# Performance work log

Hardware: AMD Instinct MI355X
Metric: run time of the kernel (lower is better)

The kernel has to match this reference:

```python
import jax, jax.numpy as jnp
import numpy as np

B, C, D = 4096, 128, 768
EPS = 1e-12
SEP = 4.0  # pair_dist in [0, 2], so 4.0 separates per-class key bands


def setup_inputs() -> dict:
    key = jax.random.key(0)
    k1, k2, k3, k4 = jax.random.split(key, 4)
    features = jax.random.normal(k1, (B, D), jnp.float32)
    centers = jax.random.normal(k2, (C, D), jnp.float32)
    labels = jax.random.randint(k3, (B,), 0, C, dtype=jnp.int32)
    cam_ids = jax.random.randint(k4, (B,), 0, 8, dtype=jnp.int32)
    return {"features": features, "centers": centers, "labels": labels, "cam_ids": cam_ids}


def _l2norm(x):
    return x / jnp.maximum(jnp.linalg.norm(x, axis=1, keepdims=True), EPS)


def reference(features, centers, labels, cam_ids):
    # cam_ids is unused by the original module.
    E = _l2norm(features)                         # [B, D] unit embeddings
    Cn = _l2norm(jax.lax.stop_gradient(centers))  # [C, D] unit centers (detached)

    S = E @ E.T                                   # [B, B] pairwise cosine (differentiable)
    EC = jnp.sum(E * Cn[labels], axis=1)          # [B] cosine(embedding_i, center_{label_i})

    li = labels[:, None]
    lj = labels[None, :]
    ar = jnp.arange(B)
    upper = ar[:, None] < ar[None, :]             # i < j (each unordered pair once)
    valid = (li == lj) & upper                    # within-class pairs

    # pair distances are computed under no_grad in torch -> stop_gradient
    pd = jax.lax.stop_gradient(1.0 - jnp.clip(S, -1.0, 1.0))  # [B, B]

    # per-class lower-median threshold via ONE global sort:
    # key = class_id * SEP + pair_dist groups pairs by class, sorted by dist within class
    m = jnp.zeros((C,), jnp.int32).at[labels].add(1)   # class sizes
    npairs = (m * (m - 1)) // 2                         # pairs per class
    key_mat = jnp.where(valid, li.astype(jnp.float32) * SEP + pd, jnp.inf)
    sorted_keys = jnp.sort(key_mat.ravel())             # [B*B]
    offs = jnp.cumsum(npairs) - npairs                  # start of each class segment
    med_idx = offs + jnp.maximum(npairs - 1, 0) // 2    # torch.median = lower median
    thr = sorted_keys[med_idx] - SEP * jnp.arange(C, dtype=jnp.float32)
    thr = jnp.where(npairs > 0, thr, jnp.inf)           # classes with <2 samples: no pairs

    sel = valid & (pd > thr[labels][:, None])           # strict > as in torch

    # random interpolation ratio (no_grad in torch)
    r = jax.lax.stop_gradient(jax.random.uniform(jax.random.key(1), (B, B), jnp.float32))

    # sampled = normalize(r*e_i + (1-r)*e_j); since ||e||=1:
    #   ||sampled_pre||^2 = r^2 + (1-r)^2 + 2 r (1-r) <e_i, e_j>
    #   <sampled, c> = (r <e_i,c> + (1-r) <e_j,c>) / ||sampled_pre||
    norm2 = r * r + (1.0 - r) * (1.0 - r) + 2.0 * r * (1.0 - r) * S
    norm = jnp.maximum(jnp.sqrt(jnp.maximum(norm2, 0.0)), EPS)
    dot = (r * EC[:, None] + (1.0 - r) * EC[None, :]) / norm
    dist = 1.0 - jnp.clip(dot, -1.0, 1.0)               # [B, B]

    # the torch loop iterates over every label occurrence, so a class with m_c
    # occurrences contributes its class loss (and pair count) m_c times
    w = m[labels].astype(jnp.float32)[:, None]          # weight per pair (left label's class)
    loss = jnp.sum(jnp.where(sel, w * dist, 0.0))
    nsamp = jnp.sum(jnp.where(sel, w, 0.0))
    return jnp.where(nsamp > 0, loss / nsamp, 0.0)
```

## Files before the change

### kernel.cpp

```cpp
#include <hip/hip_runtime.h>

#define B_ 4096
#define C_ 128
#define D_ 768
#define NT 1024
#define NW (NT/64)
#define M_MAX 96
#define P_MAX (M_MAX*(M_MAX-1)/2)
#define CK 128
#define NCH (D_/CK)
#define SROW 132
#define TILE_F (M_MAX*SROW)
#define LM2 2
#define RC 127
#define SPT ((M_MAX*(CK/4) + NT - 1)/NT)
#define LCAP 64

__device__ __forceinline__ float wave_red(float v){
#pragma unroll
  for (int o = 32; o > 0; o >>= 1) v += __shfl_down(v, o, 64);
  return v;
}
__device__ __forceinline__ float clamp1(float x){ return fminf(fmaxf(x, -1.f), 1.f); }
__device__ __forceinline__ unsigned rotl32(unsigned x, int r){ return (x << r) | (x >> (32 - r)); }
__device__ __forceinline__ float dot4(float4 a, float4 b){
  return fmaf(a.x, b.x, fmaf(a.y, b.y, fmaf(a.z, b.z, a.w * b.w)));
}

__device__ float rand_ij(unsigned n){
  const unsigned half = (unsigned)B_ * (unsigned)B_ / 2u;
  unsigned c0, c1; bool hi;
  if (n < half){ c0 = n; c1 = n + half; hi = false; }
  else         { c0 = n - half; c1 = n; hi = true; }
  const unsigned K0 = 0u, K1 = 1u, K2 = 0x1BD11BDBu;
  unsigned x0 = c0 + K0, x1 = c1 + K1;
#define TFR(r) { x0 += x1; x1 = rotl32(x1, (r)); x1 ^= x0; }
  TFR(13) TFR(15) TFR(26) TFR(6)  x0 += K1; x1 += K2 + 1u;
  TFR(17) TFR(29) TFR(16) TFR(24) x0 += K2; x1 += K0 + 2u;
  TFR(13) TFR(15) TFR(26) TFR(6)  x0 += K0; x1 += K1 + 3u;
  TFR(17) TFR(29) TFR(16) TFR(24) x0 += K1; x1 += K2 + 4u;
  TFR(13) TFR(15) TFR(26) TFR(6)  x0 += K2; x1 += K0 + 5u;
#undef TFR
  unsigned bits = hi ? x1 : x0;
  return __uint_as_float((bits >> 9) | 0x3F800000u) - 1.0f;
}

__device__ __forceinline__ void decode_pair(int p, int m, int* a_, int* b_){
  float fm = (float)(2*m - 1);
  int a = (int)((fm - sqrtf(fm*fm - 8.0f*(float)p)) * 0.5f);
  a = max(0, min(a, m - 2));
  while (a > 0 && (a*(2*m - 1 - a))/2 > p) --a;
  while (((a + 1)*(2*m - 2 - a))/2 <= p) ++a;
  *a_ = a;
  *b_ = a + 1 + (p - (a*(2*m - 1 - a))/2);
}

__device__ float dotg(const float* x, const float* y){
  float s = 0.f;
  for (int k = 0; k < D_; ++k) s = fmaf(x[k], y[k], s);
  return s;
}
__device__ float S_pair_g(const float* feat, int ga, int gb){
  const float* ra = feat + (size_t)ga * D_;
  const float* rb = feat + (size_t)gb * D_;
  float d = dotg(ra, rb);
  float na = 1.f / fmaxf(sqrtf(dotg(ra, ra)), 1e-12f);
  float nb = 1.f / fmaxf(sqrtf(dotg(rb, rb)), 1e-12f);
  return d * na * nb;
}

__global__ __launch_bounds__(NT) void k_all(
    const float* __restrict__ feat, const float* __restrict__ cent,
    const int* __restrict__ labels,
    float* __restrict__ lossv, float* __restrict__ wv,
    unsigned* __restrict__ flags, float* __restrict__ out)
{
  const int c = blockIdx.x;
  const int tid = threadIdx.x;
  const int wid = tid >> 6, lane = tid & 63;

  __shared__ int   gid_s[M_MAX];
  __shared__ int   mcount;
  __shared__ __align__(16) float tile[2 * TILE_F];
  __shared__ __align__(16) float cvec[2][CK];
  float*          Sl     = tile;
  unsigned short* fidx_s = (unsigned short*)(tile + P_MAX);
  __shared__ float selfs[M_MAX];
  __shared__ float ecs[M_MAX];
  __shared__ float cn_sh;
  __shared__ int   wcnt[NW * 64];
  __shared__ int   B0_sh, ex_sh, B1_sh, ex2_sh;
  __shared__ float thr_sh;
  __shared__ float lst[LCAP];
  __shared__ int   listn;
  __shared__ float redbuf[2 * NW];
  __shared__ int   last_sh;

  if (tid == 0) mcount = 0;
  __syncthreads();
  {
    const int4* lab4 = (const int4*)labels;
    for (int i = tid; i < B_ / 4; i += NT){
      int4 L = lab4[i];
      int base = i << 2;
      if (L.x == c){ int p = atomicAdd(&mcount, 1); if (p < M_MAX) gid_s[p] = base; }
      if (L.y == c){ int p = atomicAdd(&mcount, 1); if (p < M_MAX) gid_s[p] = base + 1; }
      if (L.z == c){ int p = atomicAdd(&mcount, 1); if (p < M_MAX) gid_s[p] = base + 2; }
      if (L.w == c){ int p = atomicAdd(&mcount, 1); if (p < M_MAX) gid_s[p] = base + 3; }
    }
  }
  __syncthreads();
  const int m = mcount;

  float lloss = 0.f, lw = 0.f;

  if (m >= 2 && m <= M_MAX){
    const int P = m * (m - 1) / 2;
    const int k0 = (P - 1) >> 1;
    const float wc = (float)m;
    const int nst = m * (CK / 4);

    const int h    = (m + 1) >> 1;
    const int Upair = h * (h + 1) / 2;
    const int hec  = (m + 2) >> 1;
    const int U    = Upair + hec;

    int c0[LM2], c1[LM2], c2[LM2], c3[LM2];
    int tAv[LM2], tBv[LM2];
    float acc[LM2][4];
    int nlay = 0;
#pragma unroll
    for (int t = 0; t < LM2; ++t){
      acc[t][0] = acc[t][1] = acc[t][2] = acc[t][3] = 0.f;
      c0[t] = c1[t] = c2[t] = c3[t] = 0; tAv[t] = 0; tBv[t] = -3;
      int u = tid + t * NT;
      if (u < U){
        nlay = t + 1;
        if (u < Upair){
          int ta = 0;
          while ((ta + 1) * h - ((ta + 1) * ta) / 2 <= u) ++ta;
          int tb = ta + (u - (ta * h - (ta * (ta - 1)) / 2));
          c0[t] = ta; c1[t] = ta + h; c2[t] = tb; c3[t] = tb + h;
          tAv[t] = ta; tBv[t] = tb;
        } else {
          int g = u - Upair;
          int l1 = g + hec;
          c0[t] = g;
          c1[t] = (l1 == m) ? RC : ((l1 < m) ? l1 : 0);
          c2[t] = RC; c3[t] = RC;
          tAv[t] = g; tBv[t] = -1;
        }
      }
    }

    float4 pf[SPT];
    float4 cpf;
#pragma unroll
    for (int k = 0; k < SPT; ++k){
      int e = tid + k * NT;
      if (e < nst){
        int r = e >> 5, j = e & 31;
        pf[k] = ((const float4*)(feat + (size_t)gid_s[r] * D_))[j];
      }
    }
    if (tid < CK/4) cpf = ((const float4*)(cent + (size_t)c * D_))[tid];
#pragma unroll
    for (int k = 0; k < SPT; ++k){
      int e = tid + k * NT;
      if (e < nst){
        int r = e >> 5, j = e & 31;
        ((float4*)&tile[r * SROW])[j] = pf[k];
      }
    }
    if (tid < CK/4) ((float4*)cvec[0])[tid] = cpf;
    __syncthreads();

    for (int ch = 0; ch < NCH; ++ch){
      const int cur = ch & 1;
      if (ch + 1 < NCH){
        const int d0 = (ch + 1) * CK;
#pragma unroll
        for (int k = 0; k < SPT; ++k){
          int e = tid + k * NT;
          if (e < nst){
            int r = e >> 5, j = e & 31;
            pf[k] = ((const float4*)(feat + (size_t)gid_s[r] * D_ + d0))[j];
          }
        }
        if (tid < CK/4) cpf = ((const float4*)(cent + (size_t)c * D_ + d0))[tid];
      }
      {
        const float* tl = tile + cur * TILE_F;
        const float4* cv4 = (const float4*)cvec[cur];
#pragma unroll
        for (int t = 0; t < LM2; ++t){
          if (t < nlay){
            const float4* A0 = (c0[t] == RC) ? cv4 : (const float4*)&tl[c0[t] * SROW];
            const float4* A1 = (c1[t] == RC) ? cv4 : (const float4*)&tl[c1[t] * SROW];
            const float4* Bp0 = (c2[t] == RC) ? cv4 : (const float4*)&tl[c2[t] * SROW];
            const float4* Bp1 = (c3[t] == RC) ? cv4 : (const float4*)&tl[c3[t] * SROW];
            float s00 = 0.f, s01 = 0.f, s10 = 0.f, s11 = 0.f;
#pragma unroll 8
            for (int j = 0; j < CK/4; ++j){
              float4 a0 = A0[j], a1 = A1[j], b0 = Bp0[j], b1 = Bp1[j];
              s00 += dot4(a0, b0); s01 += dot4(a0, b1);
              s10 += dot4(a1, b0); s11 += dot4(a1, b1);
            }
            acc[t][0] += s00; acc[t][1] += s01;
            acc[t][2] += s10; acc[t][3] += s11;
          }
        }
      }
      if (ch + 1 < NCH){
        float* tn = tile + (cur ^ 1) * TILE_F;
#pragma unroll
        for (int k = 0; k < SPT; ++k){
          int e = tid + k * NT;
          if (e < nst){
            int r = e >> 5, j = e & 31;
            ((float4*)&tn[r * SROW])[j] = pf[k];
          }
        }
        if (tid < CK/4) ((float4*)cvec[cur ^ 1])[tid] = cpf;
      }
      __syncthreads();
    }

#pragma unroll
    for (int t = 0; t < LM2; ++t){
      if (t < nlay){
        if (tBv[t] == -1){
          int g = tAv[t], l1 = g + hec;
          ecs[g] = acc[t][0];
          if (l1 == m) cn_sh = acc[t][2];
          else if (l1 < m) ecs[l1] = acc[t][2];
        } else if (tBv[t] >= 0){
          const int ta = tAv[t], tb = tBv[t];
          const int a1 = ta + h;
          if (ta == tb){
            if (ta < m) selfs[ta] = acc[t][0];
            if (a1 < m) selfs[a1] = acc[t][3];
          }
        }
      }
    }
    __syncthreads();
    if (tid == 0) listn = 0;
    if (tid < m){
      float rn  = 1.f / fmaxf(sqrtf(selfs[tid]), 1e-12f);
      float cno = 1.f / fmaxf(sqrtf(cn_sh), 1e-12f);
      selfs[tid] = rn;
      ecs[tid] = ecs[tid] * rn * cno;
    }
    __syncthreads();

    float pdq_[LM2][4];
    int   fq_[LM2][4];
#pragma unroll
    for (int t = 0; t < LM2; ++t){
#pragma unroll
      for (int s = 0; s < 4; ++s){ pdq_[t][s] = 0.f; fq_[t][s] = -1; }
      if (t < nlay && tBv[t] >= 0){
        const int ta = tAv[t], tb = tBv[t], a1 = ta + h, b1 = tb + h;
        const int  pa[4]  = { ta, ta, tb, a1 };
        const int  pb[4]  = { tb, b1, a1, b1 };
        const bool dif    = (ta != tb);
        const bool val[4] = { dif, b1 < m, dif && (a1 < m), dif && (a1 < m) && (b1 < m) };
#pragma unroll
        for (int s = 0; s < 4; ++s){
          if (val[s]){
            float S = acc[t][s] * selfs[pa[s]]; S *= selfs[pb[s]];
            float pd = 1.f - clamp1(S);
            int p = (pa[s] * (2*m - 1 - pa[s])) / 2 + (pb[s] - pa[s] - 1);
            Sl[p] = S;
            int f = min(4095, (int)(pd * 2048.f));
            fidx_s[p] = (unsigned short)f;
            pdq_[t][s] = pd; fq_[t][s] = f;
          }
        }
      }
    }
    __syncthreads();

    const int nch = (P + NT - 1) / NT;
    int cl = 0;
    for (int t = 0; t < nch; ++t){
      int p = tid + t * NT;
      int bkt = -1;
      if (p < P) bkt = fidx_s[p] >> 6;
#pragma unroll
      for (int k = 0; k < 64; ++k){
        unsigned long long msk = __ballot(bkt == k);
        if (lane == k) cl += __popcll(msk);
      }
    }
    wcnt[wid*64 + lane] = cl;
    __syncthreads();
    if (tid < 64){
      int tot = 0;
#pragma unroll
      for (int w = 0; w < NW; ++w) tot += wcnt[w*64 + tid];
      int inc = tot;
#pragma unroll
      for (int o = 1; o < 64; o <<= 1){
        int v = __shfl_up(inc, o, 64);
        if (tid >= o) inc += v;
      }
      int excl = inc - tot;
      if (excl <= k0 && k0 < inc){ B0_sh = tid; ex_sh = excl; }
    }
    __syncthreads();
    const int Bsel0 = B0_sh;
    const int kt = k0 - ex_sh;
    cl = 0;
    for (int t = 0; t < nch; ++t){
      int p = tid + t * NT;
      int bkt = -1;
      if (p < P){
        int f = fidx_s[p];
        if ((f >> 6) == Bsel0) bkt = f & 63;
      }
#pragma unroll
      for (int k = 0; k < 64; ++k){
        unsigned long long msk = __ballot(bkt == k);
        if (lane == k) cl += __popcll(msk);
      }
    }
    wcnt[wid*64 + lane] = cl;
    __syncthreads();
    if (tid < 64){
      int tot = 0;
#pragma unroll
      for (int w = 0; w < NW; ++w) tot += wcnt[w*64 + tid];
      int inc = tot;
#pragma unroll
      for (int o = 1; o < 64; o <<= 1){
        int v = __shfl_up(inc, o, 64);
        if (tid >= o) inc += v;
      }
      int excl = inc - tot;
      if (excl <= kt && kt < inc){ B1_sh = tid; ex2_sh = excl; }
    }
    __syncthreads();
    const int fsel = (Bsel0 << 6) | B1_sh;
    const int ktf  = kt - ex2_sh;

#pragma unroll
    for (int t = 0; t < LM2; ++t){
#pragma unroll
      for (int s = 0; s < 4; ++s){
        if (fq_[t][s] == fsel){
          int ix = atomicAdd(&listn, 1);
          if (ix < LCAP) lst[ix] = pdq_[t][s];
        }
      }
    }
    __syncthreads();
    const int ln = listn;
    if (ln <= LCAP){
      if (tid < ln){
        float pdp = lst[tid];
        int lt = 0, eq = 0;
        for (int j = 0; j < ln; ++j){
          float v = lst[j];
          lt += (v < pdp); eq += (v == pdp);
        }
        if (lt <= ktf && ktf < lt + eq) thr_sh = pdp;
      }
    } else {
      for (int p = tid; p < P; p += NT){
        if (fidx_s[p] == (unsigned short)fsel){
          float pdp = 1.f - clamp1(Sl[p]);
          int lt = 0, eq = 0;
          for (int q = 0; q < P; ++q){
            float pdq = 1.f - clamp1(Sl[q]);
            lt += (pdq < pdp); eq += (pdq == pdp);
          }
          if (lt <= k0 && k0 < lt + eq) thr_sh = pdp;
        }
      }
    }
    __syncthreads();
    const float thr = thr_sh;

    for (int p = tid; p < P; p += NT){
      float S = Sl[p];
      float pd = 1.f - clamp1(S);
      if (pd > thr){
        int a, b; decode_pair(p, m, &a, &b);
        int ga = gid_s[a], gb = gid_s[b];
        float ea = ecs[a], eb = ecs[b];
        int i, j; float eci, ecj;
        if (ga < gb){ i = ga; j = gb; eci = ea; ecj = eb; }
        else        { i = gb; j = ga; eci = eb; ecj = ea; }
        float r = rand_ij((unsigned)i * (unsigned)B_ + (unsigned)j);
        float omr = 1.f - r;
        float n2 = r * r + omr * omr + 2.f * r * omr * S;
        float nrm = fmaxf(sqrtf(fmaxf(n2, 0.f)), 1e-12f);
        float dt = clamp1((r * eci + omr * ecj) / nrm);
        lloss += wc * (1.f - dt);
        lw += wc;
      }
    }
  } else if (m > M_MAX){
    int* mem = (int*)Sl;
    if (tid == 0) B0_sh = 0;
    __syncthreads();
    for (int i = tid; i < B_; i += NT)
      if (labels[i] == c){ int p = atomicAdd(&B0_sh, 1); mem[p] = i; }
    __syncthreads();
    const int P = m * (m - 1) / 2;
    const int k0 = (P - 1) >> 1;
    const float wc = (float)m;
    const float* cc = cent + (size_t)c * D_;
    const float cno = 1.f / fmaxf(sqrtf(dotg(cc, cc)), 1e-12f);
    for (int p = tid; p < P; p += NT){
      int a, b; decode_pair(p, m, &a, &b);
      float pdp = 1.f - clamp1(S_pair_g(feat, mem[a], mem[b]));
      int lt = 0, eq = 0;
      for (int q = 0; q < P; ++q){
        int a2, b2; decode_pair(q, m, &a2, &b2);
        float pdq = 1.f - clamp1(S_pair_g(feat, mem[a2], mem[b2]));
        lt += (pdq < pdp); eq += (pdq == pdp);
      }
      if (lt <= k0 && k0 < lt + eq) thr_sh = pdp;
    }
    __syncthreads();
    const float thr = thr_sh;
    for (int p = tid; p < P; p += NT){
      int a, b; decode_pair(p, m, &a, &b);
      int ga = mem[a], gb = mem[b];
      float S = S_pair_g(feat, ga, gb);
      float pd = 1.f - clamp1(S);
      if (pd > thr){
        if (ga > gb){ int t2 = ga; ga = gb; gb = t2; }
        const float* ra = feat + (size_t)ga * D_;
        const float* rb = feat + (size_t)gb * D_;
        float eci = dotg(ra, cc) / fmaxf(sqrtf(dotg(ra, ra)), 1e-12f) * cno;
        float ecj = dotg(rb, cc) / fmaxf(sqrtf(dotg(rb, rb)), 1e-12f) * cno;
        float r = rand_ij((unsigned)ga * (unsigned)B_ + (unsigned)gb);
        float omr = 1.f - r;
        float n2 = r * r + omr * omr + 2.f * r * omr * S;
        float nrm = fmaxf(sqrtf(fmaxf(n2, 0.f)), 1e-12f);
        float dt = clamp1((r * eci + omr * ecj) / nrm);
        lloss += wc * (1.f - dt);
        lw += wc;
      }
    }
  }

  lloss = wave_red(lloss); lw = wave_red(lw);
  if (lane == 0){ redbuf[wid] = lloss; redbuf[NW + wid] = lw; }
  __syncthreads();
  if (tid == 0){
    float tl = 0.f, tw = 0.f;
#pragma unroll
    for (int i = 0; i < NW; ++i){ tl += redbuf[i]; tw += redbuf[NW + i]; }
    __hip_atomic_store(&lossv[c], tl, __ATOMIC_RELAXED, __HIP_MEMORY_SCOPE_AGENT);
    __hip_atomic_store(&wv[c],   tw, __ATOMIC_RELAXED, __HIP_MEMORY_SCOPE_AGENT);
    unsigned old = __hip_atomic_fetch_add(&flags[0], 1u, __ATOMIC_ACQ_REL,
                                          __HIP_MEMORY_SCOPE_AGENT);
    last_sh = ((old & 127u) == 127u) ? 1 : 0;
  }
  __syncthreads();
  if (last_sh){
    float lv = 0.f, wvv = 0.f;
    if (tid < C_){
      lv  = __hip_atomic_load(&lossv[tid], __ATOMIC_RELAXED, __HIP_MEMORY_SCOPE_AGENT);
      wvv = __hip_atomic_load(&wv[tid],   __ATOMIC_RELAXED, __HIP_MEMORY_SCOPE_AGENT);
    }
    lv = wave_red(lv); wvv = wave_red(wvv);
    if (lane == 0){ redbuf[wid] = lv; redbuf[NW + wid] = wvv; }
    __syncthreads();
    if (tid == 0){
      float l = redbuf[0] + redbuf[1];
      float w = redbuf[NW] + redbuf[NW + 1];
      out[0] = (w > 0.f) ? (l / w) : 0.f;
    }
  }
}

extern "C" void kernel_launch(void* const* d_in, const int* in_sizes, int n_in,
                              void* d_out, int out_size, void* d_ws, size_t ws_size,
                              hipStream_t stream)
{
  const float* feat   = (const float*)d_in[0];
  const float* cent   = (const float*)d_in[1];
  const int*   labels = (const int*)d_in[2];

  char* ws = (char*)d_ws;
  float*    lossv = (float*)(ws + 0);
  float*    wvv   = (float*)(ws + 512);
  unsigned* flags = (unsigned*)(ws + 1024);

  k_all<<<C_, NT, 0, stream>>>(feat, cent, labels, lossv, wvv, flags, (float*)d_out);
}
```

Baseline: 112.9 us.

## Load full feature rows into LDS at once for small classes

For classes with at most 48 members, the kernel now loads all 768-dim feature rows and the center into shared memory in one step. It then computes the Gram and center dot products in one pass, which removes the six-chunk double-buffered loop and its per-chunk barriers. The fine-bucket candidate list is now rebuilt by scanning the fidx_s array instead of being kept in per-thread registers, which frees registers. The larger shared buffer (about 148KB) may reduce occupancy, and the scan adds a pass over P entries.

```diff
diff --git a/kernel.cpp b/kernel.cpp
--- a/kernel.cpp
+++ b/kernel.cpp
@@ -15,6 +15,11 @@
 #define RC 127
 #define SPT ((M_MAX*(CK/4) + NT - 1)/NT)
 #define LCAP 64
+#define MCAP 48
+#define SROWF 772
+#define FLAT_F (MCAP*SROWF)
+#define SHP_F (FLAT_F + 768)
+#define SPTF 9
 
 __device__ __forceinline__ float wave_red(float v){
 #pragma unroll
@@ -81,10 +86,9 @@
 
   __shared__ int   gid_s[M_MAX];
   __shared__ int   mcount;
-  __shared__ __align__(16) float tile[2 * TILE_F];
-  __shared__ __align__(16) float cvec[2][CK];
-  float*          Sl     = tile;
-  unsigned short* fidx_s = (unsigned short*)(tile + P_MAX);
+  __shared__ __align__(16) float shp[SHP_F];
+  float*          Sl     = shp;
+  unsigned short* fidx_s = (unsigned short*)(shp + P_MAX);
   __shared__ float selfs[M_MAX];
   __shared__ float ecs[M_MAX];
   __shared__ float cn_sh;
@@ -118,169 +122,282 @@
     const int P = m * (m - 1) / 2;
     const int k0 = (P - 1) >> 1;
     const float wc = (float)m;
-    const int nst = m * (CK / 4);
-
     const int h    = (m + 1) >> 1;
-    const int Upair = h * (h + 1) / 2;
     const int hec  = (m + 2) >> 1;
-    const int U    = Upair + hec;
-
-    int c0[LM2], c1[LM2], c2[LM2], c3[LM2];
-    int tAv[LM2], tBv[LM2];
-    float acc[LM2][4];
-    int nlay = 0;
-#pragma unroll
-    for (int t = 0; t < LM2; ++t){
-      acc[t][0] = acc[t][1] = acc[t][2] = acc[t][3] = 0.f;
-      c0[t] = c1[t] = c2[t] = c3[t] = 0; tAv[t] = 0; tBv[t] = -3;
-      int u = tid + t * NT;
-      if (u < U){
-        nlay = t + 1;
-        if (u < Upair){
+
+    if (m <= MCAP){
+      const int Upair = h * (h + 1) / 2;
+      const int U = Upair + hec;
+      int uty = -1, ta_ = 0, tb_ = 0, g_ = 0;
+      int rc0 = 0, rc1 = 0, rc2 = 0, rc3 = 0;
+      if (tid < U){
+        if (tid < Upair){
           int ta = 0;
-          while ((ta + 1) * h - ((ta + 1) * ta) / 2 <= u) ++ta;
-          int tb = ta + (u - (ta * h - (ta * (ta - 1)) / 2));
-          c0[t] = ta; c1[t] = ta + h; c2[t] = tb; c3[t] = tb + h;
-          tAv[t] = ta; tBv[t] = tb;
+          while ((ta + 1) * h - ((ta + 1) * ta) / 2 <= tid) ++ta;
+          int tb = ta + (tid - (ta * h - (ta * (ta - 1)) / 2));
+          uty = 0; ta_ = ta; tb_ = tb;
+          rc0 = ta; rc1 = ta + h; rc2 = tb; rc3 = tb + h;
         } else {
-          int g = u - Upair;
-          int l1 = g + hec;
-          c0[t] = g;
-          c1[t] = (l1 == m) ? RC : ((l1 < m) ? l1 : 0);
-          c2[t] = RC; c3[t] = RC;
-          tAv[t] = g; tBv[t] = -1;
-        }
-      }
-    }
-
-    float4 pf[SPT];
-    float4 cpf;
-#pragma unroll
-    for (int k = 0; k < SPT; ++k){
-      int e = tid + k * NT;
-      if (e < nst){
-        int r = e >> 5, j = e & 31;
-        pf[k] = ((const float4*)(feat + (size_t)gid_s[r] * D_))[j];
-      }
-    }
-    if (tid < CK/4) cpf = ((const float4*)(cent + (size_t)c * D_))[tid];
-#pragma unroll
-    for (int k = 0; k < SPT; ++k){
-      int e = tid + k * NT;
-      if (e < nst){
-        int r = e >> 5, j = e & 31;
-        ((float4*)&tile[r * SROW])[j] = pf[k];
-      }
-    }
-    if (tid < CK/4) ((float4*)cvec[0])[tid] = cpf;
-    __syncthreads();
-
-    for (int ch = 0; ch < NCH; ++ch){
-      const int cur = ch & 1;
-      if (ch + 1 < NCH){
-        const int d0 = (ch + 1) * CK;
-#pragma unroll
-        for (int k = 0; k < SPT; ++k){
-          int e = tid + k * NT;
-          if (e < nst){
-            int r = e >> 5, j = e & 31;
-            pf[k] = ((const float4*)(feat + (size_t)gid_s[r] * D_ + d0))[j];
-          }
-        }
-        if (tid < CK/4) cpf = ((const float4*)(cent + (size_t)c * D_ + d0))[tid];
-      }
-      {
-        const float* tl = tile + cur * TILE_F;
-        const float4* cv4 = (const float4*)cvec[cur];
-#pragma unroll
-        for (int t = 0; t < LM2; ++t){
-          if (t < nlay){
-            const float4* A0 = (c0[t] == RC) ? cv4 : (const float4*)&tl[c0[t] * SROW];
-            const float4* A1 = (c1[t] == RC) ? cv4 : (const float4*)&tl[c1[t] * SROW];
-            const float4* Bp0 = (c2[t] == RC) ? cv4 : (const float4*)&tl[c2[t] * SROW];
-            const float4* Bp1 = (c3[t] == RC) ? cv4 : (const float4*)&tl[c3[t] * SROW];
-            float s00 = 0.f, s01 = 0.f, s10 = 0.f, s11 = 0.f;
+          int g = tid - Upair, l1 = g + hec;
+          uty = 2; g_ = g;
+          rc0 = g;
+          rc1 = (l1 == m) ? RC : ((l1 < m) ? l1 : 0);
+          rc2 = RC; rc3 = RC;
+        }
+      }
+
+      const int nstF = m * 192;
+      float4 st[SPTF];
+      float4 cvf;
+#pragma unroll
+      for (int k = 0; k < SPTF; ++k){
+        int e = tid + k * NT;
+        if (e < nstF){
+          int r = e / 192, j = e - r * 192;
+          st[k] = ((const float4*)(feat + (size_t)gid_s[r] * D_))[j];
+        }
+      }
+      if (tid < 192) cvf = ((const float4*)(cent + (size_t)c * D_))[tid];
+#pragma unroll
+      for (int k = 0; k < SPTF; ++k){
+        int e = tid + k * NT;
+        if (e < nstF){
+          int r = e / 192, j = e - r * 192;
+          ((float4*)&shp[r * SROWF])[j] = st[k];
+        }
+      }
+      if (tid < 192) ((float4*)(shp + FLAT_F))[tid] = cvf;
+      __syncthreads();
+
+      float a0s = 0.f, a1s = 0.f, a2s = 0.f, a3s = 0.f;
+      if (uty >= 0){
+        const float4* cv4 = (const float4*)(shp + FLAT_F);
+        const float4* A0 = (rc0 == RC) ? cv4 : (const float4*)&shp[rc0 * SROWF];
+        const float4* A1 = (rc1 == RC) ? cv4 : (const float4*)&shp[rc1 * SROWF];
+        const float4* Bp0 = (rc2 == RC) ? cv4 : (const float4*)&shp[rc2 * SROWF];
+        const float4* Bp1 = (rc3 == RC) ? cv4 : (const float4*)&shp[rc3 * SROWF];
+        for (int ch = 0; ch < NCH; ++ch){
+          const int q0 = ch * 32;
+          float s00 = 0.f, s01 = 0.f, s10 = 0.f, s11 = 0.f;
 #pragma unroll 8
-            for (int j = 0; j < CK/4; ++j){
-              float4 a0 = A0[j], a1 = A1[j], b0 = Bp0[j], b1 = Bp1[j];
-              s00 += dot4(a0, b0); s01 += dot4(a0, b1);
-              s10 += dot4(a1, b0); s11 += dot4(a1, b1);
+          for (int j = 0; j < 32; ++j){
+            float4 a0 = A0[q0 + j], a1 = A1[q0 + j];
+            float4 b0 = Bp0[q0 + j], b1 = Bp1[q0 + j];
+            s00 += dot4(a0, b0); s01 += dot4(a0, b1);
+            s10 += dot4(a1, b0); s11 += dot4(a1, b1);
+          }
+          a0s += s00; a1s += s01; a2s += s10; a3s += s11;
+        }
+      }
+
+      if (uty == 0){
+        if (ta_ == tb_){
+          if (ta_ < m) selfs[ta_] = a0s;
+          if (ta_ + h < m) selfs[ta_ + h] = a3s;
+        }
+      } else if (uty == 2){
+        ecs[g_] = a0s;
+        int l1 = g_ + hec;
+        if (l1 == m) cn_sh = a2s;
+        else if (l1 < m) ecs[l1] = a2s;
+      }
+      __syncthreads();
+      if (tid == 0) listn = 0;
+      if (tid < m){
+        float rn  = 1.f / fmaxf(sqrtf(selfs[tid]), 1e-12f);
+        float cno = 1.f / fmaxf(sqrtf(cn_sh), 1e-12f);
+        selfs[tid] = rn;
+        ecs[tid] = ecs[tid] * rn * cno;
+      }
+      __syncthreads();
+
+      if (uty == 0){
+        const int a1r = ta_ + h, b1r = tb_ + h;
+        const bool dif = (ta_ != tb_);
+        if (dif){
+          float S = a0s * selfs[ta_]; S *= selfs[tb_];
+          float pd = 1.f - clamp1(S);
+          int p = (ta_*(2*m - 1 - ta_))/2 + (tb_ - ta_ - 1);
+          Sl[p] = S; fidx_s[p] = (unsigned short)min(4095, (int)(pd * 2048.f));
+        }
+        if (b1r < m){
+          float S = a1s * selfs[ta_]; S *= selfs[b1r];
+          float pd = 1.f - clamp1(S);
+          int p = (ta_*(2*m - 1 - ta_))/2 + (b1r - ta_ - 1);
+          Sl[p] = S; fidx_s[p] = (unsigned short)min(4095, (int)(pd * 2048.f));
+        }
+        if (dif && a1r < m){
+          float S = a2s * selfs[tb_]; S *= selfs[a1r];
+          float pd = 1.f - clamp1(S);
+          int p = (tb_*(2*m - 1 - tb_))/2 + (a1r - tb_ - 1);
+          Sl[p] = S; fidx_s[p] = (unsigned short)min(4095, (int)(pd * 2048.f));
+        }
+        if (dif && a1r < m && b1r < m){
+          float S = a3s * selfs[a1r]; S *= selfs[b1r];
+          float pd = 1.f - clamp1(S);
+          int p = (a1r*(2*m - 1 - a1r))/2 + (b1r - a1r - 1);
+          Sl[p] = S; fidx_s[p] = (unsigned short)min(4095, (int)(pd * 2048.f));
+        }
+      }
+      __syncthreads();
+    } else {
+      const int nst = m * (CK / 4);
+      float* tile = shp;
+      float (*cvec)[CK] = (float(*)[CK])(shp + 2 * TILE_F);
+      const int Upair = h * (h + 1) / 2;
+      const int U = Upair + hec;
+
+      int c0[LM2], c1[LM2], c2[LM2], c3[LM2];
+      int tAv[LM2], tBv[LM2];
+      float acc[LM2][4];
+      int nlay = 0;
+#pragma unroll
+      for (int t = 0; t < LM2; ++t){
+        acc[t][0] = acc[t][1] = acc[t][2] = acc[t][3] = 0.f;
+        c0[t] = c1[t] = c2[t] = c3[t] = 0; tAv[t] = 0; tBv[t] = -3;
+        int u = tid + t * NT;
+        if (u < U){
+          nlay = t + 1;
+          if (u < Upair){
+            int ta = 0;
+            while ((ta + 1) * h - ((ta + 1) * ta) / 2 <= u) ++ta;
+            int tb = ta + (u - (ta * h - (ta * (ta - 1)) / 2));
+            c0[t] = ta; c1[t] = ta + h; c2[t] = tb; c3[t] = tb + h;
+            tAv[t] = ta; tBv[t] = tb;
+          } else {
+            int g = u - Upair;
+            int l1 = g + hec;
+            c0[t] = g;
+            c1[t] = (l1 == m) ? RC : ((l1 < m) ? l1 : 0);
+            c2[t] = RC; c3[t] = RC;
+            tAv[t] = g; tBv[t] = -1;
+          }
+        }
+      }
+
+      float4 pf[SPT];
+      float4 cpf;
+#pragma unroll
+      for (int k = 0; k < SPT; ++k){
+        int e = tid + k * NT;
+        if (e < nst){
+          int r = e >> 5, j = e & 31;
+          pf[k] = ((const float4*)(feat + (size_t)gid_s[r] * D_))[j];
+        }
+      }
+      if (tid < CK/4) cpf = ((const float4*)(cent + (size_t)c * D_))[tid];
+#pragma unroll
+      for (int k = 0; k < SPT; ++k){
+        int e = tid + k * NT;
+        if (e < nst){
+          int r = e >> 5, j = e & 31;
+          ((float4*)&tile[r * SROW])[j] = pf[k];
+        }
+      }
+      if (tid < CK/4) ((float4*)cvec[0])[tid] = cpf;
+      __syncthreads();
+
+      for (int ch = 0; ch < NCH; ++ch){
+        const int cur = ch & 1;
+        if (ch + 1 < NCH){
+          const int d0 = (ch + 1) * CK;
+#pragma unroll
+          for (int k = 0; k < SPT; ++k){
+            int e = tid + k * NT;
+            if (e < nst){
+              int r = e >> 5, j = e & 31;
+              pf[k] = ((const float4*)(feat + (size_t)gid_s[r] * D_ + d0))[j];
             }
-            acc[t][0] += s00; acc[t][1] += s01;
-            acc[t][2] += s10; acc[t][3] += s11;
-          }
-        }
-      }
-      if (ch + 1 < NCH){
-        float* tn = tile + (cur ^ 1) * TILE_F;
-#pragma unroll
-        for (int k = 0; k < SPT; ++k){
-          int e = tid + k * NT;
-          if (e < nst){
-            int r = e >> 5, j = e & 31;
-            ((float4*)&tn[r * SROW])[j] = pf[k];
-          }
-        }
-        if (tid < CK/4) ((float4*)cvec[cur ^ 1])[tid] = cpf;
-      }
-      __syncthreads();
-    }
-
-#pragma unroll
-    for (int t = 0; t < LM2; ++t){
-      if (t < nlay){
-        if (tBv[t] == -1){
-          int g = tAv[t], l1 = g + hec;
-          ecs[g] = acc[t][0];
-          if (l1 == m) cn_sh = acc[t][2];
-          else if (l1 < m) ecs[l1] = acc[t][2];
-        } else if (tBv[t] >= 0){
-          const int ta = tAv[t], tb = tBv[t];
-          const int a1 = ta + h;
-          if (ta == tb){
-            if (ta < m) selfs[ta] = acc[t][0];
-            if (a1 < m) selfs[a1] = acc[t][3];
-          }
-        }
-      }
-    }
-    __syncthreads();
-    if (tid == 0) listn = 0;
-    if (tid < m){
-      float rn  = 1.f / fmaxf(sqrtf(selfs[tid]), 1e-12f);
-      float cno = 1.f / fmaxf(sqrtf(cn_sh), 1e-12f);
-      selfs[tid] = rn;
-      ecs[tid] = ecs[tid] * rn * cno;
-    }
-    __syncthreads();
-
-    float pdq_[LM2][4];
-    int   fq_[LM2][4];
-#pragma unroll
-    for (int t = 0; t < LM2; ++t){
-#pragma unroll
-      for (int s = 0; s < 4; ++s){ pdq_[t][s] = 0.f; fq_[t][s] = -1; }
-      if (t < nlay && tBv[t] >= 0){
-        const int ta = tAv[t], tb = tBv[t], a1 = ta + h, b1 = tb + h;
-        const int  pa[4]  = { ta, ta, tb, a1 };
-        const int  pb[4]  = { tb, b1, a1, b1 };
-        const bool dif    = (ta != tb);
-        const bool val[4] = { dif, b1 < m, dif && (a1 < m), dif && (a1 < m) && (b1 < m) };
-#pragma unroll
-        for (int s = 0; s < 4; ++s){
-          if (val[s]){
-            float S = acc[t][s] * selfs[pa[s]]; S *= selfs[pb[s]];
-            float pd = 1.f - clamp1(S);
-            int p = (pa[s] * (2*m - 1 - pa[s])) / 2 + (pb[s] - pa[s] - 1);
-            Sl[p] = S;
-            int f = min(4095, (int)(pd * 2048.f));
-            fidx_s[p] = (unsigned short)f;
-            pdq_[t][s] = pd; fq_[t][s] = f;
-          }
-        }
-      }
-    }
-    __syncthreads();
+          }
+          if (tid < CK/4) cpf = ((const float4*)(cent + (size_t)c * D_ + d0))[tid];
+        }
+        {
+          const float* tl = tile + cur * TILE_F;
+          const float4* cv4 = (const float4*)cvec[cur];
+#pragma unroll
+          for (int t = 0; t < LM2; ++t){
+            if (t < nlay){
+              const float4* A0 = (c0[t] == RC) ? cv4 : (const float4*)&tl[c0[t] * SROW];
+              const float4* A1 = (c1[t] == RC) ? cv4 : (const float4*)&tl[c1[t] * SROW];
+              const float4* Bp0 = (c2[t] == RC) ? cv4 : (const float4*)&tl[c2[t] * SROW];
+              const float4* Bp1 = (c3[t] == RC) ? cv4 : (const float4*)&tl[c3[t] * SROW];
+              float s00 = 0.f, s01 = 0.f, s10 = 0.f, s11 = 0.f;
+#pragma unroll 8
+              for (int j = 0; j < CK/4; ++j){
+                float4 a0 = A0[j], a1 = A1[j], b0 = Bp0[j], b1 = Bp1[j];
+                s00 += dot4(a0, b0); s01 += dot4(a0, b1);
+                s10 += dot4(a1, b0); s11 += dot4(a1, b1);
+              }
+              acc[t][0] += s00; acc[t][1] += s01;
+              acc[t][2] += s10; acc[t][3] += s11;
+            }
+          }
+        }
+        if (ch + 1 < NCH){
+          float* tn = tile + (cur ^ 1) * TILE_F;
+#pragma unroll
+          for (int k = 0; k < SPT; ++k){
+            int e = tid + k * NT;
+            if (e < nst){
+              int r = e >> 5, j = e & 31;
+              ((float4*)&tn[r * SROW])[j] = pf[k];
+            }
+          }
+          if (tid < CK/4) ((float4*)cvec[cur ^ 1])[tid] = cpf;
+        }
+        __syncthreads();
+      }
+
+#pragma unroll
+      for (int t = 0; t < LM2; ++t){
+        if (t < nlay){
+          if (tBv[t] == -1){
+            int g = tAv[t], l1 = g + hec;
+            ecs[g] = acc[t][0];
+            if (l1 == m) cn_sh = acc[t][2];
+            else if (l1 < m) ecs[l1] = acc[t][2];
+          } else if (tBv[t] >= 0){
+            const int ta = tAv[t], tb = tBv[t];
+            const int a1 = ta + h;
+            if (ta == tb){
+              if (ta < m) selfs[ta] = acc[t][0];
+              if (a1 < m) selfs[a1] = acc[t][3];
+            }
+          }
+        }
+      }
+      __syncthreads();
+      if (tid == 0) listn = 0;
+      if (tid < m){
+        float rn  = 1.f / fmaxf(sqrtf(selfs[tid]), 1e-12f);
+        float cno = 1.f / fmaxf(sqrtf(cn_sh), 1e-12f);
+        selfs[tid] = rn;
+        ecs[tid] = ecs[tid] * rn * cno;
+      }
+      __syncthreads();
+
+#pragma unroll
+      for (int t = 0; t < LM2; ++t){
+        if (t < nlay && tBv[t] >= 0){
+          const int ta = tAv[t], tb = tBv[t], a1 = ta + h, b1 = tb + h;
+          const int  pa[4]  = { ta, ta, tb, a1 };
+          const int  pb[4]  = { tb, b1, a1, b1 };
+          const bool dif    = (ta != tb);
+          const bool val[4] = { dif, b1 < m, dif && (a1 < m), dif && (a1 < m) && (b1 < m) };
+#pragma unroll
+          for (int s = 0; s < 4; ++s){
+            if (val[s]){
+              float S = acc[t][s] * selfs[pa[s]]; S *= selfs[pb[s]];
+              float pd = 1.f - clamp1(S);
+              int p = (pa[s] * (2*m - 1 - pa[s])) / 2 + (pb[s] - pa[s] - 1);
+              Sl[p] = S;
+              fidx_s[p] = (unsigned short)min(4095, (int)(pd * 2048.f));
+            }
+          }
+        }
+      }
+      __syncthreads();
+    }
 
     const int nch = (P + NT - 1) / NT;
     int cl = 0;
@@ -345,14 +462,10 @@
     const int fsel = (Bsel0 << 6) | B1_sh;
     const int ktf  = kt - ex2_sh;
 
-#pragma unroll
-    for (int t = 0; t < LM2; ++t){
-#pragma unroll
-      for (int s = 0; s < 4; ++s){
-        if (fq_[t][s] == fsel){
-          int ix = atomicAdd(&listn, 1);
-          if (ix < LCAP) lst[ix] = pdq_[t][s];
-        }
+    for (int p = tid; p < P; p += NT){
+      if (fidx_s[p] == (unsigned short)fsel){
+        int ix = atomicAdd(&listn, 1);
+        if (ix < LCAP) lst[ix] = 1.f - clamp1(Sl[p]);
       }
     }
     __syncthreads();
```

Result: faster. 103.6 us (median of 2 runs) (-8.2%).
